# Optimization experiments

Hardware: AMD Instinct MI355X
Metric: run time of the kernel (lower is better)

The kernel has to match this reference:

```python
import jax, jax.numpy as jnp
import numpy as np

C = 256
CQ = C // 4


def setup_inputs() -> dict:
    key = jax.random.key(0)
    ks = jax.random.split(key, 7)
    B, H, W = 4, 64, 64
    x = jax.random.normal(ks[0], (B, C, H, W), dtype=jnp.float32)
    s = 1.0 / np.sqrt(C)
    Wq = jax.random.normal(ks[1], (CQ, C), dtype=jnp.float32) * s
    bq = jnp.zeros((CQ,), dtype=jnp.float32)
    Wk = jax.random.normal(ks[2], (CQ, C), dtype=jnp.float32) * s
    bk = jnp.zeros((CQ,), dtype=jnp.float32)
    Wv = jax.random.normal(ks[3], (C, C), dtype=jnp.float32) * s
    bv = jnp.zeros((C,), dtype=jnp.float32)
    gamma = jnp.zeros((1,), dtype=jnp.float32)
    return {"x": x, "Wq": Wq, "bq": bq, "Wk": Wk, "bk": bk,
            "Wv": Wv, "bv": bv, "gamma": gamma}


def reference(x, Wq, bq, Wk, bk, Wv, bv, gamma):
    B, Cc, Hh, Ww = x.shape
    N = Hh * Ww
    xf = x.reshape(B, Cc, N)                      # [B, C, N]
    # 1x1 convs are channel-mixing matmuls
    q = jnp.einsum('oc,bcn->bon', Wq, xf) + bq[None, :, None]   # [B, C/4, N]
    k = jnp.einsum('oc,bcn->bon', Wk, xf) + bk[None, :, None]   # [B, C/4, N]
    v = jnp.einsum('oc,bcn->bon', Wv, xf) + bv[None, :, None]   # [B, C, N]
    energy = jnp.einsum('bci,bcj->bij', q, k)     # [B, N, N] (unscaled)
    attn = jax.nn.softmax(energy, axis=-1)
    out = jnp.einsum('bcj,bij->bci', v, attn)     # [B, C, N]
    out = out.reshape(B, Cc, Hh, Ww)
    return gamma[0] * out + x
```

## Files before the change

### kernel.cpp

```cpp
#include <hip/hip_runtime.h>
#include <hip/hip_bf16.h>

typedef unsigned short u16;
typedef unsigned int u32;
typedef float f32x4 __attribute__((ext_vector_type(4)));
typedef short s16x8 __attribute__((ext_vector_type(8)));

#define MFMA16(a, b, c) __builtin_amdgcn_mfma_f32_16x16x32_bf16(a, b, c, 0, 0, 0)

#define NN 4096
#define CC 256
#define CQ 64

__device__ __forceinline__ u16 f2bf(float x) {
    union { float f; u32 u; } v; v.f = x;
    return (u16)((v.u + 0x7FFFu + ((v.u >> 16) & 1u)) >> 16);
}
__device__ __forceinline__ float bf2f(u16 u) {
    union { u32 u; float f; } v; v.u = ((u32)u) << 16;
    return v.f;
}
__device__ __forceinline__ void gll16(const void* g, void* l) {
    __builtin_amdgcn_global_load_lds(
        (const __attribute__((address_space(1))) void*)g,
        (__attribute__((address_space(3))) void*)l, 16, 0, 0);
}

__global__ __launch_bounds__(256) void prep(
    const float* __restrict__ x, const float* __restrict__ Wq,
    const float* __restrict__ Wk, const float* __restrict__ Wv,
    u16* __restrict__ xT, u16* __restrict__ wbf)
{
    const int bid = blockIdx.x, t = threadIdx.x;
    if (bid < 1024) {
        __shared__ float tile[64 * 65];
        const int b = bid >> 8, ctile = (bid >> 6) & 3, ntile = bid & 63;
        const int c0 = ctile * 64, n0 = ntile * 64;
        const int cw = t >> 4, nj = (t & 15) * 4;
        for (int it = 0; it < 4; it++) {
            const int ci = it * 16 + cw;
            const float4 v4 = *(const float4*)(x + ((size_t)(b * CC + c0 + ci)) * NN + n0 + nj);
            tile[(nj + 0) * 65 + ci] = v4.x;
            tile[(nj + 1) * 65 + ci] = v4.y;
            tile[(nj + 2) * 65 + ci] = v4.z;
            tile[(nj + 3) * 65 + ci] = v4.w;
        }
        __syncthreads();
        const int r = t >> 2, c16 = (t & 3) * 16;
        union { u16 h[16]; uint4 q[2]; } pk;
        for (int j = 0; j < 16; j++) pk.h[j] = f2bf(tile[r * 65 + c16 + j]);
        u16* dst = xT + ((size_t)(b * NN + n0 + r)) * CC + c0 + c16;
        *(uint4*)dst = pk.q[0];
        *(uint4*)(dst + 8) = pk.q[1];
    } else {
        const int flat = (bid - 1024) * 1024 + t * 4;
        const int o = flat >> 8, c = flat & 255;
        const float* src = (o < 64)  ? (Wq + (size_t)o * CC + c)
                         : (o < 128) ? (Wk + (size_t)(o - 64) * CC + c)
                                     : (Wv + (size_t)(o - 128) * CC + c);
        const float4 v4 = *(const float4*)src;
        union { u16 h[4]; uint2 d; } pk;
        pk.h[0] = f2bf(v4.x); pk.h[1] = f2bf(v4.y);
        pk.h[2] = f2bf(v4.z); pk.h[3] = f2bf(v4.w);
        *(uint2*)(wbf + (size_t)o * CC + c) = pk.d;
    }
}

__global__ __launch_bounds__(512, 4) void qkv(
    const u16* __restrict__ xT, const u16* __restrict__ wbf,
    const float* __restrict__ bq, const float* __restrict__ bk,
    const float* __restrict__ bv,
    u16* __restrict__ qT, u16* __restrict__ kT, u16* __restrict__ v)
{
    __shared__ __align__(16) u16 sm[384 * 64 + 32 * 64];
    u16* Ws = sm;
    u16* Xs = sm + 384 * 64;

    const int bid = blockIdx.x;
    const int b = bid >> 7, n0 = (bid & 127) * 32;
    const int t = threadIdx.x, lane = t & 63, w = t >> 6;
    const int col = lane & 15, quad = lane >> 4;

    f32x4 acc[3][2];
    for (int i = 0; i < 3; i++) { acc[i][0] = f32x4{0,0,0,0}; acc[i][1] = f32x4{0,0,0,0}; }

    for (int cc = 0; cc < 4; cc++) {
        const int c0 = cc * 64;
        for (int m = 0; m < 6; m++) {
            const int g = m * 512 + t;
            const int row = g >> 3, ch = g & 7;
            gll16(wbf + (size_t)row * CC + c0 + ((ch ^ (row & 7)) * 8), Ws + g * 8);
        }
        if (w < 4) {
            const int g = w * 64 + lane;
            const int n = g >> 3, ch = g & 7;
            gll16(xT + ((size_t)(b * NN + n0 + n)) * CC + c0 + ((ch ^ (n & 7)) * 8),
                  Xs + g * 8);
        }
        __syncthreads();
        for (int kk = 0; kk < 2; kk++) {
            s16x8 bx[2];
            for (int nt2 = 0; nt2 < 2; nt2++) {
                const int n = nt2 * 16 + col;
                bx[nt2] = *(const s16x8*)&Xs[n * 64 + (((kk * 4 + quad) ^ (n & 7)) * 8)];
            }
            for (int ot = 0; ot < 3; ot++) {
                const int row = w * 48 + ot * 16 + col;
                const s16x8 a = *(const s16x8*)&Ws[row * 64 + (((kk * 4 + quad) ^ (row & 7)) * 8)];
                acc[ot][0] = MFMA16(a, bx[0], acc[ot][0]);
                acc[ot][1] = MFMA16(a, bx[1], acc[ot][1]);
            }
        }
        __syncthreads();
    }
    for (int ot = 0; ot < 3; ot++) {
        const int og = w * 48 + ot * 16 + quad * 4;
        for (int nt2 = 0; nt2 < 2; nt2++) {
            const int n = n0 + nt2 * 16 + col;
            if (og < 64) {
                union { u16 h[4]; uint2 d; } pk;
                for (int r = 0; r < 4; r++) pk.h[r] = f2bf(acc[ot][nt2][r] + bq[og + r]);
                *(uint2*)(qT + ((size_t)(b * NN + n)) * CQ + og) = pk.d;
            } else if (og < 128) {
                union { u16 h[4]; uint2 d; } pk;
                for (int r = 0; r < 4; r++) pk.h[r] = f2bf(acc[ot][nt2][r] + bk[og - 64 + r]);
                *(uint2*)(kT + ((size_t)(b * NN + n)) * CQ + (og - 64)) = pk.d;
            } else {
                for (int r = 0; r < 4; r++)
                    v[((size_t)(b * CC + og - 128 + r)) * NN + n] =
                        f2bf(acc[ot][nt2][r] + bv[og - 128 + r]);
            }
        }
    }
}

__global__ __launch_bounds__(512, 4) void flash_attn(
    const u16* __restrict__ qT, const u16* __restrict__ kT,
    const u16* __restrict__ v,
    u16* __restrict__ Op0, float* __restrict__ Op1,
    float* __restrict__ lws)
{
    __shared__ __align__(16) u16 sm[25600];
    __shared__ float ls[2][64];

    const int bid = blockIdx.x;
    const int p = bid & 7;
    const int b = p >> 1, jh = p & 1;
    const int n0 = (bid >> 3) * 64;
    const int jb = jh * 2048;
    const int t = threadIdx.x;
    const int lane = t & 63, wv = t >> 6;
    const int col = lane & 15, quad = lane >> 4;
    const int strip = wv & 3, jhi = wv >> 2;
    const int ih = wv >> 2, cq = wv & 3;

    s16x8 aq[2];
    {
        const u16* qp = qT + ((size_t)(b * NN + n0 + strip * 16 + col)) * CQ + quad * 8;
        aq[0] = *(const s16x8*)qp;
        aq[1] = *(const s16x8*)(qp + 32);
    }

    f32x4 o_[2][4];
    for (int i = 0; i < 2; i++) for (int j = 0; j < 4; j++) o_[i][j] = f32x4{0,0,0,0};
    float lac[4] = {0.f, 0.f, 0.f, 0.f};

    const int kg = wv * 64 + lane;
    const int krow = kg >> 3;
    const u16* ksrc = kT + ((size_t)(b * NN + jb + krow)) * CQ + (((kg & 7) ^ (krow & 7)) * 8);
    const int kdo = kg * 8;
    const u16* vsrc[2];
    int vdo[2];
    for (int m = 0; m < 2; m++) {
        const int g = m * 512 + t;
        const int row = g >> 2;
        vdo[m] = g * 8;
        vsrc[m] = v + ((size_t)(b * CC + row)) * NN + jb + (g & 3) * 8;
    }

    auto issueK = [&](int jt, int kb) {
        if (wv < 4) gll16(ksrc + (size_t)jt * 32 * CQ, sm + kb * 2048 + kdo);
    };
    auto issueV = [&](int jt, int vb) {
        u16* base = sm + 4096 + vb * 8192;
        for (int m = 0; m < 2; m++)
            gll16(vsrc[m] + jt * 32, base + vdo[m]);
    };
    auto S_phase = [&](int kb, int pb) {
        const u16* Kb = sm + kb * 2048;
        u16* Pb = sm + 20480 + pb * 2560;
        f32x4 s = f32x4{0,0,0,0};
        for (int kk = 0; kk < 2; kk++) {
            const int jrow = jhi * 16 + col;
            const s16x8 bk_ = *(const s16x8*)
                &Kb[jrow * 64 + (((kk * 4 + quad) ^ (jrow & 7)) * 8)];
            s = MFMA16(aq[kk], bk_, s);
        }
        for (int r = 0; r < 4; r++) {
            const float pv = __expf(fminf(s[r], 60.f));
            lac[r] += pv;
            Pb[(strip * 16 + quad * 4 + r) * 40 + jhi * 16 + col] = f2bf(pv);
        }
    };
    auto PV_phase = [&](int pb, int vb) {
        const u16* Pb = sm + 20480 + pb * 2560;
        const u16* Vb = sm + 4096 + vb * 8192;
        s16x8 pa[2];
        for (int it2 = 0; it2 < 2; it2++)
            pa[it2] = *(const s16x8*)&Pb[((ih * 2 + it2) * 16 + col) * 40 + quad * 8];
        for (int ct = 0; ct < 4; ct++) {
            const int c = cq * 64 + ct * 16 + col;
            const s16x8 bv_ = *(const s16x8*)&Vb[c * 32 + quad * 8];
            o_[0][ct] = MFMA16(pa[0], bv_, o_[0][ct]);
            o_[1][ct] = MFMA16(pa[1], bv_, o_[1][ct]);
        }
    };

    issueK(0, 0);
    issueV(0, 0);
    issueK(1, 1);
    __syncthreads();
    S_phase(0, 0);

    int vcur = 0, pcur = 0;
    for (int m = 0; m < 64; m++) {
        __syncthreads();
        issueV((m + 1 < 64) ? m + 1 : 63, vcur ^ 1);
        issueK((m + 2 < 64) ? m + 2 : 63, m & 1);
        PV_phase(pcur, vcur);
        if (m < 63) S_phase((m + 1) & 1, pcur ^ 1);
        vcur ^= 1; pcur ^= 1;
    }

    for (int r = 0; r < 4; r++) {
        float lv = lac[r];
        lv += __shfl_xor(lv, 1, 64);
        lv += __shfl_xor(lv, 2, 64);
        lv += __shfl_xor(lv, 4, 64);
        lv += __shfl_xor(lv, 8, 64);
        lac[r] = lv;
    }
    if (col == 0)
        for (int r = 0; r < 4; r++)
            ls[jhi][strip * 16 + quad * 4 + r] = lac[r];
    __syncthreads();
    if (t < 64)
        lws[(size_t)jh * 4 * NN + (size_t)b * NN + n0 + t] = ls[0][t] + ls[1][t];

    float* Tf = (float*)sm;
    u16*  Tu = sm;
    for (int rd = 0; rd < 2; rd++) {
        if ((cq >> 1) == rd) {
            const int cl = (cq & 1) * 64;
            for (int it2 = 0; it2 < 2; it2++) {
                const int ib = (ih * 2 + it2) * 16 + quad * 4;
                for (int ct = 0; ct < 4; ct++) {
                    const int c = cl + ct * 16 + col;
                    if (jh == 0) {
                        union { u16 h[4]; uint2 d; } pk;
                        for (int r = 0; r < 4; r++) pk.h[r] = f2bf(o_[it2][ct][r]);
                        *(uint2*)&Tu[c * 136 + ib] = pk.d;
                    } else {
                        *(float2*)&Tf[c * 68 + ib] = float2{o_[it2][ct][0], o_[it2][ct][1]};
                        *(float2*)&Tf[c * 68 + ib + 2] = float2{o_[it2][ct][2], o_[it2][ct][3]};
                    }
                }
            }
        }
        __syncthreads();
        const int cl = t >> 2, i0 = (t & 3) * 16;
        const int c = rd * 128 + cl;
        if (jh == 0) {
            u16* dst = Op0 + ((size_t)(b * CC + c)) * NN + n0 + i0;
            *(uint4*)dst       = *(const uint4*)&Tu[cl * 136 + i0];
            *(uint4*)(dst + 8) = *(const uint4*)&Tu[cl * 136 + i0 + 8];
        } else {
            float* dst = Op1 + ((size_t)(b * CC + c)) * NN + n0 + i0;
            for (int k = 0; k < 4; k++)
                *(float4*)(dst + k * 4) = *(const float4*)&Tf[cl * 68 + i0 + k * 4];
        }
        __syncthreads();
    }
}

__global__ __launch_bounds__(256) void combine(
    const float* __restrict__ x, const u16* __restrict__ Op0,
    const float* __restrict__ lws, const float* __restrict__ gamma,
    float* __restrict__ out)
{
    const size_t idx = ((size_t)blockIdx.x * 256 + threadIdx.x) * 4;
    const int b = (int)(idx >> 20);
    const int n = (int)(idx & (NN - 1));
    const float g = gamma[0];
    const float4 xv = *(const float4*)(x + idx);
    const float4 o1 = *(const float4*)(out + idx);
    const u16* o0p = Op0 + idx;
    const float4 l0 = *(const float4*)(lws + (size_t)b * NN + n);
    const float4 l1 = *(const float4*)(lws + (size_t)4 * NN + (size_t)b * NN + n);
    float4 r;
    r.x = xv.x + g * (bf2f(o0p[0]) + o1.x) / (l0.x + l1.x);
    r.y = xv.y + g * (bf2f(o0p[1]) + o1.y) / (l0.y + l1.y);
    r.z = xv.z + g * (bf2f(o0p[2]) + o1.z) / (l0.z + l1.z);
    r.w = xv.w + g * (bf2f(o0p[3]) + o1.w) / (l0.w + l1.w);
    *(float4*)(out + idx) = r;
}

extern "C" void kernel_launch(void* const* d_in, const int* in_sizes, int n_in,
                              void* d_out, int out_size, void* d_ws, size_t ws_size,
                              hipStream_t stream)
{
    const float* x     = (const float*)d_in[0];
    const float* Wq    = (const float*)d_in[1];
    const float* bq    = (const float*)d_in[2];
    const float* Wk    = (const float*)d_in[3];
    const float* bk    = (const float*)d_in[4];
    const float* Wv    = (const float*)d_in[5];
    const float* bv    = (const float*)d_in[6];
    const float* gamma = (const float*)d_in[7];
    float* out = (float*)d_out;

    u16* xT  = (u16*)d_ws;
    u16* wbf = xT  + (size_t)4 * NN * CC;
    u16* qTw = wbf + (size_t)384 * CC;
    u16* kTw = qTw + (size_t)4 * NN * CQ;
    u16* vw  = kTw + (size_t)4 * NN * CQ;
    u16* Op0 = xT;
    float* lws = (float*)wbf;

    prep<<<1120, 256, 0, stream>>>(x, Wq, Wk, Wv, xT, wbf);
    qkv<<<512, 512, 0, stream>>>(xT, wbf, bq, bk, bv, qTw, kTw, vw);
    flash_attn<<<512, 512, 0, stream>>>(qTw, kTw, vw, Op0, out, lws);
    combine<<<4096, 256, 0, stream>>>(x, Op0, lws, gamma, out);
}
```

Before: 169.9 us.

## Use 128-row query tiles with four-way key split and swizzled V LDS

Flash-attention blocks now cover 128 query rows instead of 64, and the key range is split into four quarters instead of two. Grid size stays the same, and each loaded K/V tile now feeds twice as many MFMAs, which halves K/V traffic per query row. The change also XOR-swizzles the V layout in LDS to avoid bank conflicts, and packs P pairs via DPP into 32-bit stores. In exchange there are more accumulator registers, more LDS, and two extra bf16 partial-output buffers that the combine kernel must read.

```diff
diff --git a/kernel.cpp b/kernel.cpp
--- a/kernel.cpp
+++ b/kernel.cpp
@@ -24,6 +24,12 @@
     __builtin_amdgcn_global_load_lds(
         (const __attribute__((address_space(1))) void*)g,
         (__attribute__((address_space(3))) void*)l, 16, 0, 0);
+}
+__device__ __forceinline__ float dpp_xor1(float x) {
+    union { float f; int i; } a, r;
+    a.f = x;
+    r.i = __builtin_amdgcn_mov_dpp(a.i, 0xB1, 0xF, 0xF, true);
+    return r.f;
 }
 
 __global__ __launch_bounds__(256) void prep(
@@ -137,33 +143,38 @@
 __global__ __launch_bounds__(512, 4) void flash_attn(
     const u16* __restrict__ qT, const u16* __restrict__ kT,
     const u16* __restrict__ v,
-    u16* __restrict__ Op0, float* __restrict__ Op1,
-    float* __restrict__ lws)
-{
-    __shared__ __align__(16) u16 sm[25600];
-    __shared__ float ls[2][64];
+    u16* __restrict__ Op0, u16* __restrict__ Op1, u16* __restrict__ Op2,
+    float* __restrict__ lws, float* __restrict__ out)
+{
+    __shared__ __align__(16) u16 sm[30720];
+    __shared__ float ls[256];
 
     const int bid = blockIdx.x;
     const int p = bid & 7;
-    const int b = p >> 1, jh = p & 1;
-    const int n0 = (bid >> 3) * 64;
-    const int jb = jh * 2048;
+    const int b = p >> 1;
+    const int inner = bid >> 3;
+    const int qt = inner >> 1;
+    const int jq = (p & 1) * 2 + (inner & 1);
+    const int n0 = qt * 128;
+    const int jb = jq * 1024;
     const int t = threadIdx.x;
     const int lane = t & 63, wv = t >> 6;
     const int col = lane & 15, quad = lane >> 4;
-    const int strip = wv & 3, jhi = wv >> 2;
+    const int strip0 = wv & 3, jhi = wv >> 2;
     const int ih = wv >> 2, cq = wv & 3;
-
-    s16x8 aq[2];
-    {
-        const u16* qp = qT + ((size_t)(b * NN + n0 + strip * 16 + col)) * CQ + quad * 8;
-        aq[0] = *(const s16x8*)qp;
-        aq[1] = *(const s16x8*)(qp + 32);
-    }
-
-    f32x4 o_[2][4];
-    for (int i = 0; i < 2; i++) for (int j = 0; j < 4; j++) o_[i][j] = f32x4{0,0,0,0};
-    float lac[4] = {0.f, 0.f, 0.f, 0.f};
+    const int key2 = (col >> 1) & 3;
+
+    s16x8 aq[2][2];
+    for (int st = 0; st < 2; st++) {
+        const int row = n0 + (strip0 + st * 4) * 16 + col;
+        const u16* qp = qT + ((size_t)(b * NN + row)) * CQ + quad * 8;
+        aq[st][0] = *(const s16x8*)qp;
+        aq[st][1] = *(const s16x8*)(qp + 32);
+    }
+
+    f32x4 o_[4][4];
+    for (int i = 0; i < 4; i++) for (int j = 0; j < 4; j++) o_[i][j] = f32x4{0,0,0,0};
+    float lac[2][4] = {{0.f,0.f,0.f,0.f},{0.f,0.f,0.f,0.f}};
 
     const int kg = wv * 64 + lane;
     const int krow = kg >> 3;
@@ -174,8 +185,9 @@
     for (int m = 0; m < 2; m++) {
         const int g = m * 512 + t;
         const int row = g >> 2;
+        const int chc = (g & 3) ^ ((row >> 1) & 3);
         vdo[m] = g * 8;
-        vsrc[m] = v + ((size_t)(b * CC + row)) * NN + jb + (g & 3) * 8;
+        vsrc[m] = v + ((size_t)(b * CC + row)) * NN + jb + chc * 8;
     }
 
     auto issueK = [&](int jt, int kb) {
@@ -188,31 +200,40 @@
     };
     auto S_phase = [&](int kb, int pb) {
         const u16* Kb = sm + kb * 2048;
-        u16* Pb = sm + 20480 + pb * 2560;
-        f32x4 s = f32x4{0,0,0,0};
+        u16* Pb = sm + 20480 + pb * 5120;
+        f32x4 s[2] = { f32x4{0,0,0,0}, f32x4{0,0,0,0} };
         for (int kk = 0; kk < 2; kk++) {
             const int jrow = jhi * 16 + col;
             const s16x8 bk_ = *(const s16x8*)
                 &Kb[jrow * 64 + (((kk * 4 + quad) ^ (jrow & 7)) * 8)];
-            s = MFMA16(aq[kk], bk_, s);
-        }
-        for (int r = 0; r < 4; r++) {
-            const float pv = __expf(fminf(s[r], 60.f));
-            lac[r] += pv;
-            Pb[(strip * 16 + quad * 4 + r) * 40 + jhi * 16 + col] = f2bf(pv);
+            s[0] = MFMA16(aq[0][kk], bk_, s[0]);
+            s[1] = MFMA16(aq[1][kk], bk_, s[1]);
+        }
+        for (int st = 0; st < 2; st++) {
+            const int prow = (strip0 + st * 4) * 16 + quad * 4;
+            for (int r = 0; r < 4; r++) {
+                const float pv = __expf(fminf(s[st][r], 60.f));
+                lac[st][r] += pv;
+                const float nb = dpp_xor1(pv);
+                if ((col & 1) == 0) {
+                    union { __hip_bfloat162 h; u32 u; } pk;
+                    pk.h = __float22bfloat162_rn(float2{pv, nb});
+                    *(u32*)&Pb[(prow + r) * 40 + jhi * 16 + col] = pk.u;
+                }
+            }
         }
     };
     auto PV_phase = [&](int pb, int vb) {
-        const u16* Pb = sm + 20480 + pb * 2560;
+        const u16* Pb = sm + 20480 + pb * 5120;
         const u16* Vb = sm + 4096 + vb * 8192;
-        s16x8 pa[2];
-        for (int it2 = 0; it2 < 2; it2++)
-            pa[it2] = *(const s16x8*)&Pb[((ih * 2 + it2) * 16 + col) * 40 + quad * 8];
+        s16x8 pa[4];
+        for (int it2 = 0; it2 < 4; it2++)
+            pa[it2] = *(const s16x8*)&Pb[(ih * 64 + it2 * 16 + col) * 40 + quad * 8];
         for (int ct = 0; ct < 4; ct++) {
             const int c = cq * 64 + ct * 16 + col;
-            const s16x8 bv_ = *(const s16x8*)&Vb[c * 32 + quad * 8];
-            o_[0][ct] = MFMA16(pa[0], bv_, o_[0][ct]);
-            o_[1][ct] = MFMA16(pa[1], bv_, o_[1][ct]);
+            const s16x8 bv_ = *(const s16x8*)&Vb[c * 32 + ((quad ^ key2) * 8)];
+            for (int it2 = 0; it2 < 4; it2++)
+                o_[it2][ct] = MFMA16(pa[it2], bv_, o_[it2][ct]);
         }
     };
 
@@ -223,61 +244,63 @@
     S_phase(0, 0);
 
     int vcur = 0, pcur = 0;
-    for (int m = 0; m < 64; m++) {
-        __syncthreads();
-        issueV((m + 1 < 64) ? m + 1 : 63, vcur ^ 1);
-        issueK((m + 2 < 64) ? m + 2 : 63, m & 1);
+    for (int m = 0; m < 32; m++) {
+        __syncthreads();
+        issueV((m + 1 < 32) ? m + 1 : 31, vcur ^ 1);
+        issueK((m + 2 < 32) ? m + 2 : 31, m & 1);
         PV_phase(pcur, vcur);
-        if (m < 63) S_phase((m + 1) & 1, pcur ^ 1);
+        if (m < 31) S_phase((m + 1) & 1, pcur ^ 1);
         vcur ^= 1; pcur ^= 1;
     }
 
-    for (int r = 0; r < 4; r++) {
-        float lv = lac[r];
-        lv += __shfl_xor(lv, 1, 64);
-        lv += __shfl_xor(lv, 2, 64);
-        lv += __shfl_xor(lv, 4, 64);
-        lv += __shfl_xor(lv, 8, 64);
-        lac[r] = lv;
-    }
+    for (int st = 0; st < 2; st++)
+        for (int r = 0; r < 4; r++) {
+            float lv = lac[st][r];
+            lv += __shfl_xor(lv, 1, 64);
+            lv += __shfl_xor(lv, 2, 64);
+            lv += __shfl_xor(lv, 4, 64);
+            lv += __shfl_xor(lv, 8, 64);
+            lac[st][r] = lv;
+        }
     if (col == 0)
-        for (int r = 0; r < 4; r++)
-            ls[jhi][strip * 16 + quad * 4 + r] = lac[r];
+        for (int st = 0; st < 2; st++)
+            for (int r = 0; r < 4; r++)
+                ls[jhi * 128 + (strip0 + st * 4) * 16 + quad * 4 + r] = lac[st][r];
     __syncthreads();
-    if (t < 64)
-        lws[(size_t)jh * 4 * NN + (size_t)b * NN + n0 + t] = ls[0][t] + ls[1][t];
-
+    if (t < 128)
+        lws[(size_t)jq * 4 * NN + (size_t)b * NN + n0 + t] = ls[t] + ls[128 + t];
+
+    u16* Opd = (jq == 0) ? Op0 : (jq == 1) ? Op1 : Op2;
+    u16*  Tu = sm;
     float* Tf = (float*)sm;
-    u16*  Tu = sm;
-    for (int rd = 0; rd < 2; rd++) {
-        if ((cq >> 1) == rd) {
-            const int cl = (cq & 1) * 64;
-            for (int it2 = 0; it2 < 2; it2++) {
-                const int ib = (ih * 2 + it2) * 16 + quad * 4;
+    for (int rd = 0; rd < 4; rd++) {
+        if (cq == rd) {
+            for (int it2 = 0; it2 < 4; it2++) {
+                const int ib = ih * 64 + it2 * 16 + quad * 4;
                 for (int ct = 0; ct < 4; ct++) {
-                    const int c = cl + ct * 16 + col;
-                    if (jh == 0) {
+                    const int cl = ct * 16 + col;
+                    if (jq < 3) {
                         union { u16 h[4]; uint2 d; } pk;
                         for (int r = 0; r < 4; r++) pk.h[r] = f2bf(o_[it2][ct][r]);
-                        *(uint2*)&Tu[c * 136 + ib] = pk.d;
+                        *(uint2*)&Tu[cl * 136 + ib] = pk.d;
                     } else {
-                        *(float2*)&Tf[c * 68 + ib] = float2{o_[it2][ct][0], o_[it2][ct][1]};
-                        *(float2*)&Tf[c * 68 + ib + 2] = float2{o_[it2][ct][2], o_[it2][ct][3]};
+                        *(float2*)&Tf[cl * 132 + ib]     = float2{o_[it2][ct][0], o_[it2][ct][1]};
+                        *(float2*)&Tf[cl * 132 + ib + 2] = float2{o_[it2][ct][2], o_[it2][ct][3]};
                     }
                 }
             }
         }
         __syncthreads();
-        const int cl = t >> 2, i0 = (t & 3) * 16;
-        const int c = rd * 128 + cl;
-        if (jh == 0) {
-            u16* dst = Op0 + ((size_t)(b * CC + c)) * NN + n0 + i0;
+        const int cl = t >> 3, i0 = (t & 7) * 16;
+        const int c = rd * 64 + cl;
+        if (jq < 3) {
+            u16* dst = Opd + ((size_t)(b * CC + c)) * NN + n0 + i0;
             *(uint4*)dst       = *(const uint4*)&Tu[cl * 136 + i0];
             *(uint4*)(dst + 8) = *(const uint4*)&Tu[cl * 136 + i0 + 8];
         } else {
-            float* dst = Op1 + ((size_t)(b * CC + c)) * NN + n0 + i0;
+            float* dst = out + ((size_t)(b * CC + c)) * NN + n0 + i0;
             for (int k = 0; k < 4; k++)
-                *(float4*)(dst + k * 4) = *(const float4*)&Tf[cl * 68 + i0 + k * 4];
+                *(float4*)(dst + k * 4) = *(const float4*)&Tf[cl * 132 + i0 + k * 4];
         }
         __syncthreads();
     }
@@ -285,6 +308,7 @@
 
 __global__ __launch_bounds__(256) void combine(
     const float* __restrict__ x, const u16* __restrict__ Op0,
+    const u16* __restrict__ Op1, const u16* __restrict__ Op2,
     const float* __restrict__ lws, const float* __restrict__ gamma,
     float* __restrict__ out)
 {
@@ -293,15 +317,27 @@
     const int n = (int)(idx & (NN - 1));
     const float g = gamma[0];
     const float4 xv = *(const float4*)(x + idx);
-    const float4 o1 = *(const float4*)(out + idx);
-    const u16* o0p = Op0 + idx;
-    const float4 l0 = *(const float4*)(lws + (size_t)b * NN + n);
-    const float4 l1 = *(const float4*)(lws + (size_t)4 * NN + (size_t)b * NN + n);
+    const float4 o3 = *(const float4*)(out + idx);
+    const u16* p0 = Op0 + idx;
+    const u16* p1 = Op1 + idx;
+    const u16* p2 = Op2 + idx;
+    float4 lsum;
+    {
+        const size_t lb = (size_t)b * NN + n;
+        const float4 l0 = *(const float4*)(lws + lb);
+        const float4 l1 = *(const float4*)(lws + (size_t)4 * NN + lb);
+        const float4 l2 = *(const float4*)(lws + (size_t)8 * NN + lb);
+        const float4 l3 = *(const float4*)(lws + (size_t)12 * NN + lb);
+        lsum.x = l0.x + l1.x + l2.x + l3.x;
+        lsum.y = l0.y + l1.y + l2.y + l3.y;
+        lsum.z = l0.z + l1.z + l2.z + l3.z;
+        lsum.w = l0.w + l1.w + l2.w + l3.w;
+    }
     float4 r;
-    r.x = xv.x + g * (bf2f(o0p[0]) + o1.x) / (l0.x + l1.x);
-    r.y = xv.y + g * (bf2f(o0p[1]) + o1.y) / (l0.y + l1.y);
-    r.z = xv.z + g * (bf2f(o0p[2]) + o1.z) / (l0.z + l1.z);
-    r.w = xv.w + g * (bf2f(o0p[3]) + o1.w) / (l0.w + l1.w);
+    r.x = xv.x + g * (bf2f(p0[0]) + bf2f(p1[0]) + bf2f(p2[0]) + o3.x) / lsum.x;
+    r.y = xv.y + g * (bf2f(p0[1]) + bf2f(p1[1]) + bf2f(p2[1]) + o3.y) / lsum.y;
+    r.z = xv.z + g * (bf2f(p0[2]) + bf2f(p1[2]) + bf2f(p2[2]) + o3.z) / lsum.z;
+    r.w = xv.w + g * (bf2f(p0[3]) + bf2f(p1[3]) + bf2f(p2[3]) + o3.w) / lsum.w;
     *(float4*)(out + idx) = r;
 }
 
@@ -321,14 +357,16 @@
 
     u16* xT  = (u16*)d_ws;
     u16* wbf = xT  + (size_t)4 * NN * CC;
-    u16* qTw = wbf + (size_t)384 * CC;
+    u16* Op1 = wbf + (size_t)384 * CC;
+    u16* Op2 = Op1 + (size_t)4 * NN * CC;
+    float* lws = (float*)(Op2 + (size_t)4 * NN * CC);
+    u16* qTw = (u16*)(lws + (size_t)16 * NN);
     u16* kTw = qTw + (size_t)4 * NN * CQ;
     u16* vw  = kTw + (size_t)4 * NN * CQ;
     u16* Op0 = xT;
-    float* lws = (float*)wbf;
 
     prep<<<1120, 256, 0, stream>>>(x, Wq, Wk, Wv, xT, wbf);
     qkv<<<512, 512, 0, stream>>>(xT, wbf, bq, bk, bv, qTw, kTw, vw);
-    flash_attn<<<512, 512, 0, stream>>>(qTw, kTw, vw, Op0, out, lws);
-    combine<<<4096, 256, 0, stream>>>(x, Op0, lws, gamma, out);
-}
+    flash_attn<<<512, 512, 0, stream>>>(qTw, kTw, vw, Op0, Op1, Op2, lws, out);
+    combine<<<4096, 256, 0, stream>>>(x, Op0, Op1, Op2, lws, gamma, out);
+}
```

New measurement: 178.2 us. 1.05x slower.
